# Kernel tuning notes

Measured on AMD Instinct MI355X. Metric: run time of the kernel, lower is better.

The kernel has to match this reference:

```python
import jax, jax.numpy as jnp
import numpy as np

LN_EPS = 1e-5

def _layernorm(x, gamma, beta):
    mu = jnp.mean(x, axis=-1, keepdims=True)
    var = jnp.var(x, axis=-1, keepdims=True)
    return (x - mu) * jax.lax.rsqrt(var + LN_EPS) * gamma + beta

def setup_inputs() -> dict:
    key = jax.random.key(0)
    ks = jax.random.split(key, 4)
    B, s, d, L = 8, 192, 512, 8
    h = 2048  # embed_dim * 2
    return {
        "lags": jax.random.normal(ks[0], (B, s, d, L), dtype=jnp.float32),
        "gamma1": jnp.ones((d,), jnp.float32),
        "beta1": jnp.zeros((d,), jnp.float32),
        "W1": jax.random.normal(ks[1], (d, h), jnp.float32) * (1.0 / np.sqrt(d)),
        "b1": jnp.zeros((h,), jnp.float32),
        "W2": jax.random.normal(ks[2], (h, d), jnp.float32) * (1.0 / np.sqrt(h)),
        "b2": jnp.zeros((d,), jnp.float32),
        "gamma3": jnp.ones((d,), jnp.float32),
        "beta3": jnp.zeros((d,), jnp.float32),
    }

def reference(lags, gamma1, beta1, W1, b1, W2, b2, gamma3, beta3):
    B, s, d, L = lags.shape
    # (B, s, d, L) -> (B, s, L, d) -> (B, S=s*L, d)
    x = jnp.transpose(lags, (0, 1, 3, 2)).reshape(B, s * L, d)
    scale = 1.0 / jnp.sqrt(jnp.asarray(d, x.dtype))
    # single-head, unprojected attention: scores = X X^T / sqrt(d)
    scores = jnp.einsum('bqd,bkd->bqk', x, x) * scale  # [B, S, S]
    attn = jax.nn.softmax(scores, axis=-1)
    attn_out = jnp.einsum('bqk,bkd->bqd', attn, x)
    q = _layernorm(x + attn_out, gamma1, beta1)
    ff = jnp.dot(jax.nn.gelu(jnp.dot(q, W1) + b1, approximate=False), W2) + b2
    out = _layernorm(q + ff, gamma3, beta3)
    # (B, S, d) -> (B, s, L, d) -> (B, s, d, L)
    return jnp.transpose(out.reshape(B, s, L, d), (0, 1, 3, 2))
```

## Files before the change

kernel.cpp:

```cpp
#include <hip/hip_runtime.h>
#include <hip/hip_bf16.h>
#include <math.h>

#define B_ 8
#define S_ 192
#define D_ 512
#define L_ 8
#define SQ 1536
#define H_ 2048
#define NROW (B_*SQ)
#define SCALE_QK 0.04419417382415922f

typedef unsigned short ushort_t;
typedef unsigned int uint_t;
typedef __attribute__((ext_vector_type(8))) short bf16x8;
typedef __attribute__((ext_vector_type(4))) float f32x4;

__device__ __forceinline__ float bfu2f(ushort_t u) { return __uint_as_float((unsigned)u << 16); }
__device__ __forceinline__ ushort_t f2bfu(float f) {
  __hip_bfloat16 h = __float2bfloat16(f);
  return *reinterpret_cast<ushort_t*>(&h);
}

__device__ __forceinline__ void gl_lds16(const ushort_t* g, ushort_t* l) {
  __builtin_amdgcn_global_load_lds(
      (const __attribute__((address_space(1))) unsigned int*)g,
      (__attribute__((address_space(3))) unsigned int*)l, 16, 0, 0);
}

__global__ __launch_bounds__(256) void k_build_x_f(const float* __restrict__ lags,
                                                   float* __restrict__ x,
                                                   ushort_t* __restrict__ x_bf) {
  __shared__ float tile[512][9];
  const int tid = threadIdx.x;
  const float* in = lags + (size_t)blockIdx.x * 4096;
  #pragma unroll
  for (int it = 0; it < 4; ++it) {
    int f = (tid + it * 256) * 4;
    float4 v = *reinterpret_cast<const float4*>(in + f);
    int k = f >> 3, l0 = f & 7;
    tile[k][l0] = v.x; tile[k][l0 + 1] = v.y; tile[k][l0 + 2] = v.z; tile[k][l0 + 3] = v.w;
  }
  __syncthreads();
  const int l = tid >> 5, kbase = tid & 31;
  const size_t r = (size_t)blockIdx.x * 8 + l;
  #pragma unroll
  for (int j = 0; j < 16; ++j) {
    int k = kbase + 32 * j;
    float v = tile[k][l];
    x[r * D_ + k] = v;
    x_bf[r * D_ + k] = f2bfu(v);
  }
}

__global__ __launch_bounds__(256) void k_xt(const ushort_t* __restrict__ x_bf,
                                            ushort_t* __restrict__ xT) {
  __shared__ ushort_t tile[64][65];
  int t0 = blockIdx.x * 64, d0 = blockIdx.y * 64;
  const ushort_t* X = x_bf + (size_t)blockIdx.z * SQ * D_;
  ushort_t* XT = xT + (size_t)blockIdx.z * SQ * D_;
  for (int i = threadIdx.x; i < 4096; i += 256) {
    int tt = i >> 6, dd = i & 63;
    tile[dd][tt] = X[(size_t)(t0 + tt) * D_ + d0 + dd];
  }
  __syncthreads();
  for (int i = threadIdx.x; i < 4096; i += 256) {
    int dd = i >> 6, tt = i & 63;
    XT[(size_t)(d0 + dd) * SQ + t0 + tt] = tile[dd][tt];
  }
}

__global__ __launch_bounds__(256) void k_wt(const float* __restrict__ W,
                                            ushort_t* __restrict__ Wt,
                                            int K, int N) {
  __shared__ ushort_t tile[64][65];
  int n0 = blockIdx.x * 64, k0 = blockIdx.y * 64;
  for (int i = threadIdx.x; i < 4096; i += 256) {
    int kk = i >> 6, nn = i & 63;
    tile[nn][kk] = f2bfu(W[(size_t)(k0 + kk) * N + n0 + nn]);
  }
  __syncthreads();
  for (int i = threadIdx.x; i < 4096; i += 256) {
    int nn = i >> 6, kk = i & 63;
    Wt[(size_t)(n0 + nn) * K + k0 + kk] = tile[nn][kk];
  }
}

template<int MODE>
__global__ __launch_bounds__(256) void k_gemm(const ushort_t* __restrict__ A,
                                              const ushort_t* __restrict__ Bt,
                                              const float* __restrict__ bias,
                                              void* __restrict__ Cout,
                                              int M, int K, int N,
                                              size_t sAz, size_t sBz, size_t sCz,
                                              float scale) {
  A  += (size_t)blockIdx.z * sAz;
  Bt += (size_t)blockIdx.z * sBz;
  __shared__ ushort_t As[128 * 32];
  __shared__ ushort_t Bs[128 * 32];
  const int tid = threadIdx.x;
  const int m0 = blockIdx.y * 128, n0 = blockIdx.x * 128;
  const int w = tid >> 6, lane = tid & 63;
  const int wr = w >> 1, wc = w & 1;
  const int l15 = lane & 15, quad = lane >> 4;
  const int srow = w * 32 + (lane >> 2);
  const int scol = (lane & 3) * 8;
  ushort_t* lA = &As[(w * 32) * 32];
  ushort_t* lB = &Bs[(w * 32) * 32];

  f32x4 acc[4][4];
  if (MODE <= 1) {
    #pragma unroll
    for (int nj = 0; nj < 4; ++nj) {
      float bv = bias[n0 + wc * 64 + nj * 16 + l15];
      #pragma unroll
      for (int mi = 0; mi < 4; ++mi) acc[mi][nj] = (f32x4){bv, bv, bv, bv};
    }
  } else {
    #pragma unroll
    for (int nj = 0; nj < 4; ++nj)
      #pragma unroll
      for (int mi = 0; mi < 4; ++mi) acc[mi][nj] = (f32x4){0.f, 0.f, 0.f, 0.f};
  }

  for (int k0 = 0; k0 < K; k0 += 32) {
    const ushort_t* gA = A  + (size_t)(m0 + srow) * K + k0 + scol;
    const ushort_t* gB = Bt + (size_t)(n0 + srow) * K + k0 + scol;
    __syncthreads();
    gl_lds16(gA, lA);
    gl_lds16(gA + (size_t)16 * K, lA + 16 * 32);
    gl_lds16(gB, lB);
    gl_lds16(gB + (size_t)16 * K, lB + 16 * 32);
    __syncthreads();
    bf16x8 af[4], bfv[4];
    #pragma unroll
    for (int mi = 0; mi < 4; ++mi)
      af[mi] = *reinterpret_cast<const bf16x8*>(&As[(wr * 64 + mi * 16 + l15) * 32 + quad * 8]);
    #pragma unroll
    for (int nj = 0; nj < 4; ++nj)
      bfv[nj] = *reinterpret_cast<const bf16x8*>(&Bs[(wc * 64 + nj * 16 + l15) * 32 + quad * 8]);
    #pragma unroll
    for (int mi = 0; mi < 4; ++mi)
      #pragma unroll
      for (int nj = 0; nj < 4; ++nj)
        acc[mi][nj] = __builtin_amdgcn_mfma_f32_16x16x32_bf16(af[mi], bfv[nj], acc[mi][nj], 0, 0, 0);
  }

  ushort_t* Cb = (ushort_t*)Cout + (size_t)blockIdx.z * sCz;
  float*    Cf = (float*)Cout    + (size_t)blockIdx.z * sCz;
  #pragma unroll
  for (int mi = 0; mi < 4; ++mi)
    #pragma unroll
    for (int nj = 0; nj < 4; ++nj) {
      int gc = n0 + wc * 64 + nj * 16 + l15;
      #pragma unroll
      for (int r = 0; r < 4; ++r) {
        int gr = m0 + wr * 64 + mi * 16 + quad * 4 + r;
        float v = acc[mi][nj][r];
        if (MODE == 0) {
          v = 0.5f * v * (1.0f + erff(v * 0.70710678118654752f));
          Cb[(size_t)gr * N + gc] = f2bfu(v);
        } else if (MODE == 1) {
          Cf[(size_t)gr * N + gc] = v;
        } else if (MODE == 2) {
          Cb[(size_t)gr * N + gc] = f2bfu(v * scale);
        } else {
          Cf[(size_t)gr * N + gc] = v;
        }
      }
    }
}

__global__ __launch_bounds__(256) void k_softmax_bf(ushort_t* __restrict__ sc) {
  uint_t* row = (uint_t*)(sc + (size_t)blockIdx.z * SQ * SQ + (size_t)blockIdx.x * SQ);
  int tid = threadIdx.x;
  __shared__ float red[8];
  float v[6];
  float m = -1e30f;
  #pragma unroll
  for (int k = 0; k < 3; ++k) {
    uint_t u = row[tid + k * 256];
    v[2*k]   = __uint_as_float(u << 16);
    v[2*k+1] = __uint_as_float(u & 0xffff0000u);
    m = fmaxf(m, fmaxf(v[2*k], v[2*k+1]));
  }
  #pragma unroll
  for (int o = 32; o > 0; o >>= 1) m = fmaxf(m, __shfl_down(m, o));
  if ((tid & 63) == 0) red[tid >> 6] = m;
  __syncthreads();
  m = fmaxf(fmaxf(red[0], red[1]), fmaxf(red[2], red[3]));
  __syncthreads();
  float ssum = 0.f;
  #pragma unroll
  for (int k = 0; k < 6; ++k) { v[k] = expf(v[k] - m); ssum += v[k]; }
  #pragma unroll
  for (int o = 32; o > 0; o >>= 1) ssum += __shfl_down(ssum, o);
  if ((tid & 63) == 0) red[4 + (tid >> 6)] = ssum;
  __syncthreads();
  float inv = 1.0f / (red[4] + red[5] + red[6] + red[7]);
  #pragma unroll
  for (int k = 0; k < 3; ++k) {
    uint_t lo = f2bfu(v[2*k] * inv);
    uint_t hi = f2bfu(v[2*k+1] * inv);
    row[tid + k * 256] = (hi << 16) | lo;
  }
}

__global__ __launch_bounds__(256) void k_ln1b(const float* __restrict__ x,
                                              const float* __restrict__ attn,
                                              const float* __restrict__ g,
                                              const float* __restrict__ be,
                                              ushort_t* __restrict__ qbf) {
  size_t base = (size_t)blockIdx.x * D_;
  int tid = threadIdx.x;
  __shared__ float rl[8];
  float v0 = x[base + tid] + attn[base + tid];
  float v1 = x[base + tid + 256] + attn[base + tid + 256];
  float s = v0 + v1, sq = v0 * v0 + v1 * v1;
  #pragma unroll
  for (int o = 32; o > 0; o >>= 1) { s += __shfl_down(s, o); sq += __shfl_down(sq, o); }
  int lane = tid & 63, wid = tid >> 6;
  if (lane == 0) { rl[wid] = s; rl[4 + wid] = sq; }
  __syncthreads();
  s = rl[0] + rl[1] + rl[2] + rl[3];
  sq = rl[4] + rl[5] + rl[6] + rl[7];
  float mean = s * (1.0f / 512.0f);
  float var = sq * (1.0f / 512.0f) - mean * mean;
  float rstd = rsqrtf(var + 1e-5f);
  qbf[base + tid]       = f2bfu((v0 - mean) * rstd * g[tid] + be[tid]);
  qbf[base + tid + 256] = f2bfu((v1 - mean) * rstd * g[tid + 256] + be[tid + 256]);
}

__global__ __launch_bounds__(256) void k_ln3_f(const float* __restrict__ y,
                                               const ushort_t* __restrict__ qbf,
                                               const float* __restrict__ g3,
                                               const float* __restrict__ be3,
                                               float* __restrict__ out) {
  __shared__ float ynorm[8][512];
  const int tid = threadIdx.x;
  const int w = tid >> 6, lane = tid & 63;
  #pragma unroll
  for (int rr = 0; rr < 2; ++rr) {
    int l = 2 * w + rr;
    size_t t = (size_t)blockIdx.x * 8 + l;
    float v[8];
    float s = 0.f, sq = 0.f;
    #pragma unroll
    for (int j = 0; j < 8; ++j) {
      int k = lane + 64 * j;
      v[j] = y[t * D_ + k] + bfu2f(qbf[t * D_ + k]);
      s += v[j]; sq += v[j] * v[j];
    }
    #pragma unroll
    for (int o = 32; o > 0; o >>= 1) { s += __shfl_down(s, o); sq += __shfl_down(sq, o); }
    s = __shfl(s, 0); sq = __shfl(sq, 0);
    float mean = s * (1.0f / 512.0f);
    float var = sq * (1.0f / 512.0f) - mean * mean;
    float rstd = rsqrtf(var + 1e-5f);
    #pragma unroll
    for (int j = 0; j < 8; ++j) {
      int k = lane + 64 * j;
      ynorm[l][k] = (v[j] - mean) * rstd * g3[k] + be3[k];
    }
  }
  __syncthreads();
  float* ob = out + (size_t)blockIdx.x * 4096;
  #pragma unroll
  for (int kk = 0; kk < 2; ++kk) {
    int k = tid * 2 + kk;
    float4 lo = make_float4(ynorm[0][k], ynorm[1][k], ynorm[2][k], ynorm[3][k]);
    float4 hi = make_float4(ynorm[4][k], ynorm[5][k], ynorm[6][k], ynorm[7][k]);
    *reinterpret_cast<float4*>(ob + (size_t)k * 8)     = lo;
    *reinterpret_cast<float4*>(ob + (size_t)k * 8 + 4) = hi;
  }
}

#define TS 64
#define KT 16
__global__ __launch_bounds__(256) void k_build_x_s(const float* __restrict__ lags,
                                                   float* __restrict__ x, int b_base) {
  int idx = blockIdx.x * 256 + threadIdx.x;
  int k = idx & (D_ - 1);
  int r = idx >> 9;
  int b = b_base + r / SQ;
  int t = r - (r / SQ) * SQ;
  int si = t >> 3, l = t & 7;
  size_t src = (((size_t)(b * S_ + si) * D_ + k) << 3) + l;
  x[idx] = lags[src];
}

__global__ __launch_bounds__(256) void k_scores(const float* __restrict__ x,
                                                float* __restrict__ sc, int b_base) {
  const float* A = x;
  float* C = sc;
  __shared__ float As[TS][KT + 1];
  __shared__ float Bs[TS][KT + 1];
  int tx = threadIdx.x & 15, ty = threadIdx.x >> 4;
  int j0 = blockIdx.x * TS, i0 = blockIdx.y * TS;
  float acc[4][4] = {};
  int lk = threadIdx.x & 15, lr = threadIdx.x >> 4;
  for (int k0 = 0; k0 < D_; k0 += KT) {
    #pragma unroll
    for (int it = 0; it < 4; ++it) {
      As[lr + 16 * it][lk] = A[(size_t)(i0 + lr + 16 * it) * D_ + k0 + lk];
      Bs[lr + 16 * it][lk] = A[(size_t)(j0 + lr + 16 * it) * D_ + k0 + lk];
    }
    __syncthreads();
    #pragma unroll
    for (int kk = 0; kk < KT; ++kk) {
      float a[4], bb[4];
      #pragma unroll
      for (int r = 0; r < 4; ++r) a[r] = As[ty * 4 + r][kk];
      #pragma unroll
      for (int c = 0; c < 4; ++c) bb[c] = Bs[tx * 4 + c][kk];
      #pragma unroll
      for (int r = 0; r < 4; ++r)
        #pragma unroll
        for (int c = 0; c < 4; ++c) acc[r][c] = fmaf(a[r], bb[c], acc[r][c]);
    }
    __syncthreads();
  }
  #pragma unroll
  for (int r = 0; r < 4; ++r) {
    float4 v = make_float4(acc[r][0]*SCALE_QK, acc[r][1]*SCALE_QK,
                           acc[r][2]*SCALE_QK, acc[r][3]*SCALE_QK);
    *reinterpret_cast<float4*>(&C[(size_t)(i0 + ty*4 + r) * SQ + j0 + tx*4]) = v;
  }
}

__global__ __launch_bounds__(256) void k_softmax(float* __restrict__ sc) {
  float* row = sc + (size_t)blockIdx.x * SQ;
  int tid = threadIdx.x;
  __shared__ float red[8];
  float m = -1e30f;
  for (int j = tid; j < SQ; j += 256) m = fmaxf(m, row[j]);
  #pragma unroll
  for (int o = 32; o > 0; o >>= 1) m = fmaxf(m, __shfl_down(m, o));
  if ((tid & 63) == 0) red[tid >> 6] = m;
  __syncthreads();
  m = fmaxf(fmaxf(red[0], red[1]), fmaxf(red[2], red[3]));
  __syncthreads();
  float ssum = 0.f;
  for (int j = tid; j < SQ; j += 256) { float e = expf(row[j] - m); row[j] = e; ssum += e; }
  #pragma unroll
  for (int o = 32; o > 0; o >>= 1) ssum += __shfl_down(ssum, o);
  if ((tid & 63) == 0) red[4 + (tid >> 6)] = ssum;
  __syncthreads();
  float inv = 1.0f / (red[4] + red[5] + red[6] + red[7]);
  for (int j = tid; j < SQ; j += 256) row[j] *= inv;
}

__global__ __launch_bounds__(256) void k_attn(const float* __restrict__ x,
                                              const float* __restrict__ sc,
                                              float* __restrict__ attn) {
  const float* X = x;
  const float* P = sc;
  float* O = attn;
  __shared__ float Ps[TS][KT + 1];
  __shared__ float Xs[KT][TS];
  int tx = threadIdx.x & 15, ty = threadIdx.x >> 4;
  int j0 = blockIdx.x * TS, i0 = blockIdx.y * TS;
  float acc[4][4] = {};
  int lk = threadIdx.x & 15, lr = threadIdx.x >> 4;
  int lc = threadIdx.x & 63, lrow = threadIdx.x >> 6;
  for (int k0 = 0; k0 < SQ; k0 += KT) {
    #pragma unroll
    for (int it = 0; it < 4; ++it)
      Ps[lr + 16 * it][lk] = P[(size_t)(i0 + lr + 16 * it) * SQ + k0 + lk];
    #pragma unroll
    for (int it = 0; it < 4; ++it)
      Xs[lrow + 4 * it][lc] = X[(size_t)(k0 + lrow + 4 * it) * D_ + j0 + lc];
    __syncthreads();
    #pragma unroll
    for (int kk = 0; kk < KT; ++kk) {
      float a[4], bb[4];
      #pragma unroll
      for (int r = 0; r < 4; ++r) a[r] = Ps[ty * 4 + r][kk];
      #pragma unroll
      for (int c = 0; c < 4; ++c) bb[c] = Xs[kk][tx * 4 + c];
      #pragma unroll
      for (int r = 0; r < 4; ++r)
        #pragma unroll
        for (int c = 0; c < 4; ++c) acc[r][c] = fmaf(a[r], bb[c], acc[r][c]);
    }
    __syncthreads();
  }
  #pragma unroll
  for (int r = 0; r < 4; ++r) {
    float4 v = make_float4(acc[r][0], acc[r][1], acc[r][2], acc[r][3]);
    *reinterpret_cast<float4*>(&O[(size_t)(i0 + ty*4 + r) * D_ + j0 + tx*4]) = v;
  }
}

__global__ __launch_bounds__(256) void k_ln1(const float* __restrict__ x,
                                             const float* __restrict__ attn,
                                             const float* __restrict__ g,
                                             const float* __restrict__ be,
                                             float* __restrict__ qout) {
  size_t base = (size_t)blockIdx.x * D_;
  int tid = threadIdx.x;
  __shared__ float rl[8];
  float v0 = x[base + tid] + attn[base + tid];
  float v1 = x[base + tid + 256] + attn[base + tid + 256];
  float s = v0 + v1, sq = v0 * v0 + v1 * v1;
  #pragma unroll
  for (int o = 32; o > 0; o >>= 1) { s += __shfl_down(s, o); sq += __shfl_down(sq, o); }
  int lane = tid & 63, wid = tid >> 6;
  if (lane == 0) { rl[wid] = s; rl[4 + wid] = sq; }
  __syncthreads();
  s = rl[0] + rl[1] + rl[2] + rl[3];
  sq = rl[4] + rl[5] + rl[6] + rl[7];
  float mean = s * (1.0f / 512.0f);
  float var = sq * (1.0f / 512.0f) - mean * mean;
  float rstd = rsqrtf(var + 1e-5f);
  qout[base + tid]       = (v0 - mean) * rstd * g[tid] + be[tid];
  qout[base + tid + 256] = (v1 - mean) * rstd * g[tid + 256] + be[tid + 256];
}

__global__ __launch_bounds__(256, 2) void k_ffn(
    const float* __restrict__ q,
    const float* __restrict__ W1, const float* __restrict__ b1,
    const float* __restrict__ W2, const float* __restrict__ b2,
    const float* __restrict__ g3, const float* __restrict__ be3,
    float* __restrict__ out, int row_base)
{
  __shared__ float qs[8][D_];
  __shared__ float mid[8][H_];
  const int tid = threadIdx.x;
  const int row0 = blockIdx.x * 8;
  for (int idx = tid; idx < 8 * D_; idx += 256)
    qs[idx >> 9][idx & (D_ - 1)] = q[(size_t)row0 * D_ + idx];
  __syncthreads();
  float acc[8][8];
  {
    float4 bA = *reinterpret_cast<const float4*>(b1 + (tid << 3));
    float4 bB = *reinterpret_cast<const float4*>(b1 + (tid << 3) + 4);
    float bv[8] = {bA.x, bA.y, bA.z, bA.w, bB.x, bB.y, bB.z, bB.w};
    #pragma unroll
    for (int jj = 0; jj < 8; ++jj)
      #pragma unroll
      for (int r = 0; r < 8; ++r) acc[jj][r] = bv[jj];
  }
  for (int k4 = 0; k4 < D_ / 4; ++k4) {
    float4 qv[8];
    #pragma unroll
    for (int r = 0; r < 8; ++r)
      qv[r] = *reinterpret_cast<const float4*>(&qs[r][k4 << 2]);
    #pragma unroll
    for (int kk = 0; kk < 4; ++kk) {
      const int k = (k4 << 2) + kk;
      float4 wA = *reinterpret_cast<const float4*>(W1 + (size_t)k * H_ + (tid << 3));
      float4 wB = *reinterpret_cast<const float4*>(W1 + (size_t)k * H_ + (tid << 3) + 4);
      float wv[8] = {wA.x, wA.y, wA.z, wA.w, wB.x, wB.y, wB.z, wB.w};
      #pragma unroll
      for (int r = 0; r < 8; ++r) {
        float qk = (kk == 0) ? qv[r].x : (kk == 1) ? qv[r].y : (kk == 2) ? qv[r].z : qv[r].w;
        #pragma unroll
        for (int jj = 0; jj < 8; ++jj) acc[jj][r] = fmaf(qk, wv[jj], acc[jj][r]);
      }
    }
  }
  #pragma unroll
  for (int jj = 0; jj < 8; ++jj)
    #pragma unroll
    for (int r = 0; r < 8; ++r) {
      float v = acc[jj][r];
      mid[r][(tid << 3) + jj] = 0.5f * v * (1.0f + erff(v * 0.70710678118654752f));
    }
  __syncthreads();
  float acc2[8][2];
  {
    float b20 = b2[tid << 1], b21 = b2[(tid << 1) + 1];
    #pragma unroll
    for (int r = 0; r < 8; ++r) { acc2[r][0] = b20; acc2[r][1] = b21; }
  }
  for (int j4 = 0; j4 < H_ / 4; ++j4) {
    float4 mv[8];
    #pragma unroll
    for (int r = 0; r < 8; ++r)
      mv[r] = *reinterpret_cast<const float4*>(&mid[r][j4 << 2]);
    #pragma unroll
    for (int kk = 0; kk < 4; ++kk) {
      const int j = (j4 << 2) + kk;
      float2 wv = *reinterpret_cast<const float2*>(W2 + (size_t)j * D_ + (tid << 1));
      #pragma unroll
      for (int r = 0; r < 8; ++r) {
        float m = (kk == 0) ? mv[r].x : (kk == 1) ? mv[r].y : (kk == 2) ? mv[r].z : mv[r].w;
        acc2[r][0] = fmaf(m, wv.x, acc2[r][0]);
        acc2[r][1] = fmaf(m, wv.y, acc2[r][1]);
      }
    }
  }
  __syncthreads();
  float* ys = &mid[0][0];
  #pragma unroll
  for (int r = 0; r < 8; ++r) {
    ys[r * D_ + (tid << 1)]     = qs[r][(tid << 1)]     + acc2[r][0];
    ys[r * D_ + (tid << 1) + 1] = qs[r][(tid << 1) + 1] + acc2[r][1];
  }
  __syncthreads();
  float g3a = g3[tid],  g3b = g3[tid + 256];
  float be3a = be3[tid], be3b = be3[tid + 256];
  float* rl = &qs[0][0];
  for (int r = 0; r < 8; ++r) {
    float v0 = ys[r * D_ + tid], v1 = ys[r * D_ + tid + 256];
    float s = v0 + v1, sq = v0 * v0 + v1 * v1;
    #pragma unroll
    for (int o = 32; o > 0; o >>= 1) { s += __shfl_down(s, o); sq += __shfl_down(sq, o); }
    int lane = tid & 63, wid = tid >> 6;
    if (lane == 0) { rl[wid] = s; rl[4 + wid] = sq; }
    __syncthreads();
    s = rl[0] + rl[1] + rl[2] + rl[3];
    sq = rl[4] + rl[5] + rl[6] + rl[7];
    __syncthreads();
    float mean = s * (1.0f / 512.0f);
    float var = sq * (1.0f / 512.0f) - mean * mean;
    float rstd = rsqrtf(var + 1e-5f);
    int t = row_base + row0 + r;
    int b = t / SQ, tt = t - b * SQ;
    int si = tt >> 3, l = tt & 7;
    size_t ob = (((size_t)(b * S_ + si) * D_) << 3) + l;
    out[ob + ((size_t)tid << 3)]         = (v0 - mean) * rstd * g3a + be3a;
    out[ob + ((size_t)(tid + 256) << 3)] = (v1 - mean) * rstd * g3b + be3b;
  }
}

extern "C" void kernel_launch(void* const* d_in, const int* in_sizes, int n_in,
                              void* d_out, int out_size, void* d_ws, size_t ws_size,
                              hipStream_t stream) {
  const float* lags   = (const float*)d_in[0];
  const float* gamma1 = (const float*)d_in[1];
  const float* beta1  = (const float*)d_in[2];
  const float* W1     = (const float*)d_in[3];
  const float* b1     = (const float*)d_in[4];
  const float* W2     = (const float*)d_in[5];
  const float* b2     = (const float*)d_in[6];
  const float* g3     = (const float*)d_in[7];
  const float* be3    = (const float*)d_in[8];
  float* out = (float*)d_out;

  float* ws = (float*)d_ws;
  const size_t NX  = (size_t)B_ * SQ * D_;
  const size_t NXB = (size_t)SQ * D_;
  const size_t NS  = (size_t)SQ * SQ;

  const size_t need_full = (3 * NX + 8 * NS) * sizeof(float);

  if (ws_size >= need_full) {
    float* x        = ws;
    float* attn     = x + NX;
    ushort_t* q_bf  = (ushort_t*)(attn + NX);
    ushort_t* w1t   = q_bf + NX;
    ushort_t* w2t   = w1t + (size_t)H_ * D_;
    ushort_t* region = w2t + (size_t)H_ * D_;
    ushort_t* sc_bf = region;
    ushort_t* x_bf  = region + 8 * NS;
    ushort_t* xT_bf = x_bf + NX;
    ushort_t* mid_bf = region;

    k_build_x_f<<<dim3(B_ * S_), 256, 0, stream>>>(lags, x, x_bf);
    k_xt<<<dim3(SQ / 64, D_ / 64, B_), 256, 0, stream>>>(x_bf, xT_bf);
    k_wt<<<dim3(H_ / 64, D_ / 64), 256, 0, stream>>>(W1, w1t, D_, H_);
    k_wt<<<dim3(D_ / 64, H_ / 64), 256, 0, stream>>>(W2, w2t, H_, D_);
    k_gemm<2><<<dim3(SQ / 128, SQ / 128, B_), 256, 0, stream>>>(
        x_bf, x_bf, nullptr, sc_bf, SQ, D_, SQ, NXB, NXB, NS, SCALE_QK);
    k_softmax_bf<<<dim3(SQ, 1, B_), 256, 0, stream>>>(sc_bf);
    k_gemm<3><<<dim3(D_ / 128, SQ / 128, B_), 256, 0, stream>>>(
        sc_bf, xT_bf, nullptr, attn, SQ, SQ, D_, NS, NXB, NXB, 1.0f);
    k_ln1b<<<dim3(NROW), 256, 0, stream>>>(x, attn, gamma1, beta1, q_bf);
    k_gemm<0><<<dim3(H_ / 128, NROW / 128, 1), 256, 0, stream>>>(
        q_bf, w1t, b1, mid_bf, NROW, D_, H_, 0, 0, 0, 1.0f);
    k_gemm<1><<<dim3(D_ / 128, NROW / 128, 1), 256, 0, stream>>>(
        mid_bf, w2t, b2, attn, NROW, H_, D_, 0, 0, 0, 1.0f);
    k_ln3_f<<<dim3(B_ * S_), 256, 0, stream>>>(attn, q_bf, g3, be3, out);
  } else {
    float* xb   = ws;
    float* sc   = xb + NXB;
    float* atb  = sc + NS;
    float* qb   = atb + NXB;
    for (int b = 0; b < B_; ++b) {
      k_build_x_s<<<dim3((unsigned)(NXB / 256)), 256, 0, stream>>>(lags, xb, b);
      k_scores<<<dim3(SQ / TS, SQ / TS, 1), 256, 0, stream>>>(xb, sc, b);
      k_softmax<<<dim3(SQ, 1, 1), 256, 0, stream>>>(sc);
      k_attn<<<dim3(D_ / TS, SQ / TS, 1), 256, 0, stream>>>(xb, sc, atb);
      k_ln1<<<dim3(SQ), 256, 0, stream>>>(xb, atb, gamma1, beta1, qb);
      k_ffn<<<dim3(SQ / 8), 256, 0, stream>>>(qb, W1, b1, W2, b2, g3, be3, out, b * SQ);
    }
  }
}
```

Measured before the change: 347.4 us.

## Double GEMM K-tile to 64 with XOR-swizzled LDS and faster GELU

The GEMM kernel now stages a 64-wide K slice per iteration instead of 32, halving the number of barrier pairs per K loop. It stores the slice in LDS with an XOR swizzle on 16-byte column groups so the fragment reads avoid bank conflicts. Separately, the exact erff-based GELU epilogue is replaced by an Abramowitz-Stegun polynomial erf approximation using a hardware reciprocal and a fast exp. This trades some accuracy in the GELU output, already rounded to bf16, and doubles the LDS footprint per block, which could reduce occupancy.

Result: faster. 306.1 us (-11.9%).

```diff
diff --git a/kernel.cpp b/kernel.cpp
--- a/kernel.cpp
+++ b/kernel.cpp
@@ -20,6 +20,20 @@
 __device__ __forceinline__ ushort_t f2bfu(float f) {
   __hip_bfloat16 h = __float2bfloat16(f);
   return *reinterpret_cast<ushort_t*>(&h);
+}
+
+__device__ __forceinline__ float gelu_fast(float x) {
+  float z = fabsf(x) * 0.70710678118654752f;
+  float t = __builtin_amdgcn_rcpf(fmaf(0.3275911f, z, 1.0f));
+  float p = fmaf(1.061405429f, t, -1.453152027f);
+  p = fmaf(p, t, 1.421413741f);
+  p = fmaf(p, t, -0.284496736f);
+  p = fmaf(p, t, 0.254829592f);
+  p = p * t;
+  float e = __expf(-z * z);
+  float erfz = fmaf(-p, e, 1.0f);
+  float s = (x >= 0.0f) ? erfz : -erfz;
+  return 0.5f * x * (1.0f + s);
 }
 
 __device__ __forceinline__ void gl_lds16(const ushort_t* g, ushort_t* l) {
@@ -96,17 +110,18 @@
                                               float scale) {
   A  += (size_t)blockIdx.z * sAz;
   Bt += (size_t)blockIdx.z * sBz;
-  __shared__ ushort_t As[128 * 32];
-  __shared__ ushort_t Bs[128 * 32];
+  __shared__ ushort_t As[128 * 64];
+  __shared__ ushort_t Bs[128 * 64];
   const int tid = threadIdx.x;
   const int m0 = blockIdx.y * 128, n0 = blockIdx.x * 128;
   const int w = tid >> 6, lane = tid & 63;
   const int wr = w >> 1, wc = w & 1;
   const int l15 = lane & 15, quad = lane >> 4;
-  const int srow = w * 32 + (lane >> 2);
-  const int scol = (lane & 3) * 8;
-  ushort_t* lA = &As[(w * 32) * 32];
-  ushort_t* lB = &Bs[(w * 32) * 32];
+  const int lrow8 = lane >> 3;
+  const int cg = ((lane & 7) ^ lrow8) * 8;
+  const int xsw = l15 & 7;
+  ushort_t* lA = &As[(w * 32) * 64];
+  ushort_t* lB = &Bs[(w * 32) * 64];
 
   f32x4 acc[4][4];
   if (MODE <= 1) {
@@ -123,27 +138,32 @@
       for (int mi = 0; mi < 4; ++mi) acc[mi][nj] = (f32x4){0.f, 0.f, 0.f, 0.f};
   }
 
-  for (int k0 = 0; k0 < K; k0 += 32) {
-    const ushort_t* gA = A  + (size_t)(m0 + srow) * K + k0 + scol;
-    const ushort_t* gB = Bt + (size_t)(n0 + srow) * K + k0 + scol;
-    __syncthreads();
-    gl_lds16(gA, lA);
-    gl_lds16(gA + (size_t)16 * K, lA + 16 * 32);
-    gl_lds16(gB, lB);
-    gl_lds16(gB + (size_t)16 * K, lB + 16 * 32);
-    __syncthreads();
-    bf16x8 af[4], bfv[4];
-    #pragma unroll
-    for (int mi = 0; mi < 4; ++mi)
-      af[mi] = *reinterpret_cast<const bf16x8*>(&As[(wr * 64 + mi * 16 + l15) * 32 + quad * 8]);
-    #pragma unroll
-    for (int nj = 0; nj < 4; ++nj)
-      bfv[nj] = *reinterpret_cast<const bf16x8*>(&Bs[(wc * 64 + nj * 16 + l15) * 32 + quad * 8]);
-    #pragma unroll
-    for (int mi = 0; mi < 4; ++mi)
+  for (int k0 = 0; k0 < K; k0 += 64) {
+    const ushort_t* gA = A  + (size_t)(m0 + w * 32 + lrow8) * K + k0 + cg;
+    const ushort_t* gB = Bt + (size_t)(n0 + w * 32 + lrow8) * K + k0 + cg;
+    __syncthreads();
+    #pragma unroll
+    for (int j = 0; j < 4; ++j) {
+      gl_lds16(gA + (size_t)(j * 8) * K, lA + j * 8 * 64);
+      gl_lds16(gB + (size_t)(j * 8) * K, lB + j * 8 * 64);
+    }
+    __syncthreads();
+    #pragma unroll
+    for (int kk = 0; kk < 2; ++kk) {
+      const int csel = ((kk * 4 + quad) ^ xsw) * 8;
+      bf16x8 af[4], bfv[4];
+      #pragma unroll
+      for (int mi = 0; mi < 4; ++mi)
+        af[mi] = *reinterpret_cast<const bf16x8*>(&As[(wr * 64 + mi * 16 + l15) * 64 + csel]);
       #pragma unroll
       for (int nj = 0; nj < 4; ++nj)
-        acc[mi][nj] = __builtin_amdgcn_mfma_f32_16x16x32_bf16(af[mi], bfv[nj], acc[mi][nj], 0, 0, 0);
+        bfv[nj] = *reinterpret_cast<const bf16x8*>(&Bs[(wc * 64 + nj * 16 + l15) * 64 + csel]);
+      #pragma unroll
+      for (int mi = 0; mi < 4; ++mi)
+        #pragma unroll
+        for (int nj = 0; nj < 4; ++nj)
+          acc[mi][nj] = __builtin_amdgcn_mfma_f32_16x16x32_bf16(af[mi], bfv[nj], acc[mi][nj], 0, 0, 0);
+    }
   }
 
   ushort_t* Cb = (ushort_t*)Cout + (size_t)blockIdx.z * sCz;
@@ -158,8 +178,7 @@
         int gr = m0 + wr * 64 + mi * 16 + quad * 4 + r;
         float v = acc[mi][nj][r];
         if (MODE == 0) {
-          v = 0.5f * v * (1.0f + erff(v * 0.70710678118654752f));
-          Cb[(size_t)gr * N + gc] = f2bfu(v);
+          Cb[(size_t)gr * N + gc] = f2bfu(gelu_fast(v));
         } else if (MODE == 1) {
           Cf[(size_t)gr * N + gc] = v;
         } else if (MODE == 2) {
```
